# Kernel optimization log

Hardware: AMD Instinct MI355X
Metric: run time of the kernel (lower is better)

Reference implementation:

```python
import jax, jax.numpy as jnp
import numpy as np

ALPHA = 1.702  # gpt-oss gated-activation alpha
LIMIT = 7.0    # gpt-oss clamp limit
E, H, I = 8, 1024, 2048
B, S = 2, 2048


def setup_inputs() -> dict:
    key = jax.random.key(0)
    ks = jax.random.split(key, 6)
    return {
        "hidden_states": jax.random.normal(ks[0], (B, S, H), dtype=jnp.float32),
        "routing_weights": jax.random.uniform(ks[1], (B * S, E), dtype=jnp.float32),
        "gate_up_proj": jax.random.normal(ks[2], (E, H, 2 * I), dtype=jnp.float32) * 0.02,
        "gate_up_proj_bias": jax.random.normal(ks[3], (E, 2 * I), dtype=jnp.float32) * 0.02,
        "down_proj": jax.random.normal(ks[4], (E, I, H), dtype=jnp.float32) * 0.02,
        "down_proj_bias": jax.random.normal(ks[5], (E, H), dtype=jnp.float32) * 0.02,
    }


def reference(hidden_states, routing_weights, gate_up_proj, gate_up_proj_bias,
              down_proj, down_proj_bias):
    b, s, h = hidden_states.shape
    x = hidden_states.reshape(-1, h)  # [T, H]
    # all-experts dense path: [E, T, 2I]
    gate_up = jnp.einsum('th,ehd->etd', x, gate_up_proj) + gate_up_proj_bias[:, None, :]
    gate = gate_up[..., ::2]   # interleaved gate/up as in gpt-oss
    up = gate_up[..., 1::2]
    gate = jnp.minimum(gate, LIMIT)
    up = jnp.clip(up, -LIMIT, LIMIT)
    glu = gate * jax.nn.sigmoid(gate * ALPHA)
    # [E, T, H]
    out_e = jnp.einsum('eti,eih->eth', (up + 1.0) * glu, down_proj) + down_proj_bias[:, None, :]
    # weighted sum over experts with routing weights [T, E]
    out = jnp.einsum('eth,te->th', out_e, routing_weights)
    return out.reshape(b, s, h)
```

## Files before the change

### kernel.cpp

```cpp
#include <hip/hip_runtime.h>
#include <cstdint>

#define E_  8
#define H_  1024
#define I_  2048
#define T_  4096
#define D2_ 4096
#define K2_ 16384

typedef __bf16 bf16x8 __attribute__((ext_vector_type(8)));
typedef float  f32x4  __attribute__((ext_vector_type(4)));

__device__ __forceinline__ unsigned short f2bf(float f) {
  unsigned int u = __float_as_uint(f);
  u += 0x7FFFu + ((u >> 16) & 1u);
  return (unsigned short)(u >> 16);
}

__device__ __forceinline__ void gll16(const void* g, void* l) {
  __builtin_amdgcn_global_load_lds(
      (const __attribute__((address_space(1))) unsigned int*)(uintptr_t)g,
      (__attribute__((address_space(3))) unsigned int*)(uintptr_t)l,
      16, 0, 0);
}

#define BARX()  __builtin_amdgcn_s_barrier()
#define WLG()   { asm volatile("s_waitcnt lgkmcnt(0)" ::: "memory"); __builtin_amdgcn_sched_barrier(0); }
#define WVM4()  asm volatile("s_waitcnt vmcnt(4)" ::: "memory")
#define WVM0()  asm volatile("s_waitcnt vmcnt(0)" ::: "memory")

__global__ void cast_x_kernel(const float* __restrict__ x,
                              unsigned short* __restrict__ xb) {
  const int idx = (blockIdx.x * 256 + threadIdx.x) * 8;
  float4 a = *(const float4*)(x + idx);
  float4 b = *(const float4*)(x + idx + 4);
  unsigned short o[8];
  o[0]=f2bf(a.x); o[1]=f2bf(a.y); o[2]=f2bf(a.z); o[3]=f2bf(a.w);
  o[4]=f2bf(b.x); o[5]=f2bf(b.y); o[6]=f2bf(b.z); o[7]=f2bf(b.w);
  *(uint4*)(xb + idx) = *(const uint4*)o;
}

__global__ void transp_w1_kernel(const float* __restrict__ gup,
                                 unsigned short* __restrict__ w1g,
                                 unsigned short* __restrict__ w1u) {
  __shared__ float tile[64][65];
  const int h0 = blockIdx.x * 64;
  const int d0 = blockIdx.y * 64;
  const int e  = blockIdx.z;
  const int tid = threadIdx.x;
  const int r  = tid >> 4;
  const int c4 = (tid & 15) * 4;
  const float* src = gup + ((size_t)e * H_ + h0) * D2_ + d0;
#pragma unroll
  for (int c = 0; c < 4; ++c) {
    const int row = r + 16 * c;
    float4 v = *(const float4*)(src + (size_t)row * D2_ + c4);
    tile[row][c4+0] = v.x; tile[row][c4+1] = v.y;
    tile[row][c4+2] = v.z; tile[row][c4+3] = v.w;
  }
  __syncthreads();
  const int hl = tid & 63;
  const int jg = tid >> 6;
  const size_t jbase = (size_t)e * I_ + (d0 >> 1);
#pragma unroll
  for (int jj = 0; jj < 8; ++jj) {
    const int jl = jg * 8 + jj;
    w1g[(jbase + jl) * H_ + h0 + hl] = f2bf(tile[hl][2*jl]);
    w1u[(jbase + jl) * H_ + h0 + hl] = f2bf(tile[hl][2*jl+1]);
  }
}

__global__ void transp_w2_kernel(const float* __restrict__ dp,
                                 unsigned short* __restrict__ w2t) {
  __shared__ float tile[64][65];
  const int k0 = blockIdx.x * 64;
  const int h0 = blockIdx.y * 64;
  const int tid = threadIdx.x;
  const int r  = tid >> 4;
  const int c4 = (tid & 15) * 4;
#pragma unroll
  for (int c = 0; c < 4; ++c) {
    const int row = r + 16 * c;
    float4 v = *(const float4*)(dp + (size_t)(k0 + row) * H_ + h0 + c4);
    tile[row][c4+0] = v.x; tile[row][c4+1] = v.y;
    tile[row][c4+2] = v.z; tile[row][c4+3] = v.w;
  }
  __syncthreads();
  const int kl = tid & 63;
  const int hg = tid >> 6;
#pragma unroll
  for (int hh = 0; hh < 16; ++hh) {
    const int hl = hg * 16 + hh;
    w2t[(size_t)(h0 + hl) * K2_ + k0 + kl] = f2bf(tile[kl][hl]);
  }
}


#define STA1(B, HF, KT) {                                                    \
  _Pragma("unroll")                                                           \
  for (int ld = 0; ld < 2; ++ld) {                                            \
    const int r = rA + (HF)*64 + ld*128;                                      \
    gll16(Ag + (size_t)r * H_ + (KT)*64 + sg, &lds[B][r*64 + sl]);            \
  } }
#define STG1(B, KT) {                                                         \
  _Pragma("unroll")                                                           \
  for (int ld = 0; ld < 2; ++ld) {                                            \
    const int r = rA + ld*64;                                                 \
    gll16(Gg + (size_t)r * H_ + (KT)*64 + sg, &lds[B][16384 + r*64 + sl]);    \
  } }
#define STU1(B, KT) {                                                         \
  _Pragma("unroll")                                                           \
  for (int ld = 0; ld < 2; ++ld) {                                            \
    const int r = rA + ld*64;                                                 \
    gll16(Ug + (size_t)r * H_ + (KT)*64 + sg, &lds[B][24576 + r*64 + sl]);    \
  } }
#define LDA1(B, MH) {                                                         \
  _Pragma("unroll")                                                           \
  for (int m = 0; m < 4; ++m) {                                               \
    const int ro = (wm*128 + (MH)*64 + m*16 + arow) * 64;                     \
    av[m][0] = *(const bf16x8*)&lds[B][ro + sw0];                             \
    av[m][1] = *(const bf16x8*)&lds[B][ro + sw1];                             \
  } }
#define LDB1(B, DST, BASE) {                                                  \
  _Pragma("unroll")                                                           \
  for (int n = 0; n < 2; ++n) {                                               \
    const int ro = (BASE) + (wn*32 + n*16 + arow) * 64;                       \
    DST[n][0] = *(const bf16x8*)&lds[B][ro + sw0];                            \
    DST[n][1] = *(const bf16x8*)&lds[B][ro + sw1];                            \
  } }
#define MMA1(ACC, MH, BV)                                                     \
  __builtin_amdgcn_s_setprio(1);                                              \
  _Pragma("unroll")                                                           \
  for (int m = 0; m < 4; ++m)                                                 \
  _Pragma("unroll")                                                           \
  for (int n = 0; n < 2; ++n) {                                               \
    ACC[(MH)*4+m][n] = __builtin_amdgcn_mfma_f32_16x16x32_bf16(av[m][0], BV[n][0], ACC[(MH)*4+m][n], 0,0,0); \
    ACC[(MH)*4+m][n] = __builtin_amdgcn_mfma_f32_16x16x32_bf16(av[m][1], BV[n][1], ACC[(MH)*4+m][n], 0,0,0); \
  }                                                                           \
  __builtin_amdgcn_s_setprio(0);

#define NT1 16
#define TILE1(B, U) {                                                         \
    \
  LDA1(B, 0); LDB1(B, bgv, 16384); LDB1(B, buv, 24576);                       \
  if ((U)+1 < NT1) { STA1((B)^1, 1, (U)+1); STG1((B)^1, (U)+1); }             \
  WLG();                                                                      \
  MMA1(accg, 0, bgv); MMA1(accu, 0, buv);                                     \
  BARX();                                                                     \
   \
  LDA1(B, 1);                                                                 \
  if ((U)+2 < NT1) { STA1(B, 0, (U)+2); STU1(B, (U)+2); }                     \
  WLG();                                                                      \
  MMA1(accu, 1, buv); MMA1(accg, 1, bgv);                                     \
  if ((U)+2 < NT1) { WVM4(); } else { WVM0(); }                               \
  BARX();                                                                     \
}

__global__ __launch_bounds__(512, 2) void gemm1_act_kernel(
    const unsigned short* __restrict__ xb,
    const unsigned short* __restrict__ w1g,
    const unsigned short* __restrict__ w1u,
    const float* __restrict__ gub,
    const float* __restrict__ rw,
    unsigned short* __restrict__ actW)
{
  __shared__ unsigned short lds[2][32768];
  const int tid  = threadIdx.x;
  const int lane = tid & 63;
  const int wv   = tid >> 6;
  const int wm   = wv >> 2;
  const int wn   = wv & 3;

  const int L  = blockIdx.x + 16 * blockIdx.y;
  const int xk = L & 7, xs = L >> 3;
  const int t0 = ((xk >> 1) * 4 + (xs & 3)) * 256;
  const int j0 = ((xk & 1) * 8 + (xs >> 2)) * 128;
  const int e  = blockIdx.z;

  const int arow = lane & 15;
  const int q    = lane >> 4;
  const int sw0  = ((q    ) ^ (arow & 7)) * 8;
  const int sw1  = ((q + 4) ^ (arow & 7)) * 8;
  const int sg   = ((tid & 7) ^ ((tid >> 3) & 7)) * 8;
  const int sl   = (tid & 7) * 8;
  const int rA   = tid >> 3;

  const unsigned short* Ag = xb  + (size_t)t0 * H_;
  const unsigned short* Gg = w1g + ((size_t)e * I_ + j0) * H_;
  const unsigned short* Ug = w1u + ((size_t)e * I_ + j0) * H_;

  const f32x4 zero = {0.f, 0.f, 0.f, 0.f};
  f32x4 accg[8][2], accu[8][2];
#pragma unroll
  for (int m = 0; m < 8; ++m)
#pragma unroll
    for (int n = 0; n < 2; ++n) { accg[m][n] = zero; accu[m][n] = zero; }
  bf16x8 av[4][2], bgv[2][2], buv[2][2];

  STA1(0, 0, 0); STU1(0, 0); STA1(0, 1, 0); STG1(0, 0);
  STA1(1, 0, 1); STU1(1, 1);
  WVM4(); BARX();

#pragma unroll 1
  for (int t = 0; t < NT1; t += 2) {
    TILE1(0, t);
    TILE1(1, t+1);
  }

  const float* gbE = gub + (size_t)e * D2_;
#pragma unroll
  for (int n = 0; n < 2; ++n) {
    const int j = j0 + wn*32 + n*16 + arow;
    const float2 bgu = *(const float2*)&gbE[2*j];
#pragma unroll
    for (int mf = 0; mf < 8; ++mf) {
#pragma unroll
      for (int ri = 0; ri < 4; ++ri) {
        const int t = t0 + wm*128 + mf*16 + q*4 + ri;
        float g = accg[mf][n][ri] + bgu.x;
        float u = accu[mf][n][ri] + bgu.y;
        g = fminf(g, 7.0f);
        u = fminf(fmaxf(u, -7.0f), 7.0f);
        const float s   = 1.0f / (1.0f + __expf(-1.702f * g));
        const float val = (u + 1.0f) * (g * s) * rw[t * 8 + e];
        actW[(size_t)t * K2_ + e * I_ + j] = f2bf(val);
      }
    }
  }
}


#define STA2(B, HF, KT) {                                                    \
  _Pragma("unroll")                                                           \
  for (int ld = 0; ld < 2; ++ld) {                                            \
    const int r = rA + (HF)*64 + ld*128;                                      \
    gll16(Ag + (size_t)r * K2_ + (KT)*64 + sg, &lds[B][r*64 + sl]);           \
  } }
#define STB2(B, NH, KT) {                                                    \
  _Pragma("unroll")                                                           \
  for (int ld = 0; ld < 2; ++ld) {                                            \
    const int lr = rA + ld*64;                                                \
    const int r  = (lr & 31) + (NH)*32 + ((lr >> 5) << 6);                    \
    gll16(Bgp + (size_t)r * K2_ + (KT)*64 + sg, &lds[B][16384 + r*64 + sl]);  \
  } }
#define LDA2(B, MH) {                                                         \
  _Pragma("unroll")                                                           \
  for (int m = 0; m < 4; ++m) {                                               \
    const int ro = (wm*128 + (MH)*64 + m*16 + arow) * 64;                     \
    av[m][0] = *(const bf16x8*)&lds[B][ro + sw0];                             \
    av[m][1] = *(const bf16x8*)&lds[B][ro + sw1];                             \
  } }
#define LDB2(B, DST, NH) {                                                   \
  _Pragma("unroll")                                                           \
  for (int n = 0; n < 2; ++n) {                                               \
    const int ro = 16384 + (wn*64 + (NH)*32 + n*16 + arow) * 64;              \
    DST[n][0] = *(const bf16x8*)&lds[B][ro + sw0];                            \
    DST[n][1] = *(const bf16x8*)&lds[B][ro + sw1];                            \
  } }
#define MMA2(MH, NH, BV)                                                      \
  __builtin_amdgcn_s_setprio(1);                                              \
  _Pragma("unroll")                                                           \
  for (int m = 0; m < 4; ++m)                                                 \
  _Pragma("unroll")                                                           \
  for (int n = 0; n < 2; ++n) {                                               \
    acc[(MH)*4+m][(NH)*2+n] = __builtin_amdgcn_mfma_f32_16x16x32_bf16(av[m][0], BV[n][0], acc[(MH)*4+m][(NH)*2+n], 0,0,0); \
    acc[(MH)*4+m][(NH)*2+n] = __builtin_amdgcn_mfma_f32_16x16x32_bf16(av[m][1], BV[n][1], acc[(MH)*4+m][(NH)*2+n], 0,0,0); \
  }                                                                           \
  __builtin_amdgcn_s_setprio(0);

#define NT2 64
#define TILE2(B, U) {                                                         \
  LDA2(B, 0); LDB2(B, bv0, 0); LDB2(B, bv1, 1);                               \
  if ((U)+1 < NT2) { STA2((B)^1, 1, (U)+1); STB2((B)^1, 0, (U)+1); }          \
  WLG();                                                                      \
  MMA2(0, 0, bv0); MMA2(0, 1, bv1);                                           \
  BARX();                                                                     \
  LDA2(B, 1);                                                                 \
  if ((U)+2 < NT2) { STA2(B, 0, (U)+2); STB2(B, 1, (U)+2); }                  \
  WLG();                                                                      \
  MMA2(1, 1, bv1); MMA2(1, 0, bv0);                                           \
  if ((U)+2 < NT2) { WVM4(); } else { WVM0(); }                               \
  BARX();                                                                     \
}

__global__ __launch_bounds__(512, 2) void gemm2_kernel(
    const unsigned short* __restrict__ actW,
    const unsigned short* __restrict__ w2t,
    float* __restrict__ part)
{
  __shared__ unsigned short lds[2][32768];
  const int tid  = threadIdx.x;
  const int lane = tid & 63;
  const int wv   = tid >> 6;
  const int wm   = wv >> 2;
  const int wn   = wv & 3;

  const int L  = blockIdx.x + 16 * (blockIdx.y + 4 * blockIdx.z);
  const int xk = L & 7, xs = L >> 3;
  const int t0 = ((xk & 1) * 8 + (xs & 7)) * 256;
  const int h0 = (xs >> 3) * 256;
  const int cz = xk >> 1;
  const int c0 = cz * 4096;

  const int arow = lane & 15;
  const int q    = lane >> 4;
  const int sw0  = ((q    ) ^ (arow & 7)) * 8;
  const int sw1  = ((q + 4) ^ (arow & 7)) * 8;
  const int sg   = ((tid & 7) ^ ((tid >> 3) & 7)) * 8;
  const int sl   = (tid & 7) * 8;
  const int rA   = tid >> 3;

  const unsigned short* Ag  = actW + (size_t)t0 * K2_ + c0;
  const unsigned short* Bgp = w2t  + (size_t)h0 * K2_ + c0;

  const f32x4 zero = {0.f, 0.f, 0.f, 0.f};
  f32x4 acc[8][4];
#pragma unroll
  for (int m = 0; m < 8; ++m)
#pragma unroll
    for (int n = 0; n < 4; ++n) acc[m][n] = zero;
  bf16x8 av[4][2], bv0[2][2], bv1[2][2];

  STA2(0, 0, 0); STB2(0, 1, 0); STA2(0, 1, 0); STB2(0, 0, 0);
  STA2(1, 0, 1); STB2(1, 1, 1);
  WVM4(); BARX();

#pragma unroll 1
  for (int t = 0; t < NT2; t += 2) {
    TILE2(0, t);
    TILE2(1, t+1);
  }

  float* P = part + (size_t)cz * ((size_t)T_ * H_);
#pragma unroll
  for (int mf = 0; mf < 8; ++mf)
#pragma unroll
    for (int nf = 0; nf < 4; ++nf)
#pragma unroll
      for (int ri = 0; ri < 4; ++ri) {
        const int t = t0 + wm*128 + mf*16 + q*4 + ri;
        const int h = h0 + wn*64 + nf*16 + arow;
        P[(size_t)t * H_ + h] = acc[mf][nf][ri];
      }
}

__global__ void reduce_kernel(const float* __restrict__ part,
                              const float* __restrict__ rw,
                              const float* __restrict__ dpb,
                              float* __restrict__ out) {
  const int idx = blockIdx.x * 256 + threadIdx.x;
  const int t  = idx >> 8;
  const int hq = idx & 255;
  const float4* p = (const float4*)part;
  float4 v = p[idx];
  float4 a;
  a = p[idx + 1048576]; v.x += a.x; v.y += a.y; v.z += a.z; v.w += a.w;
  a = p[idx + 2097152]; v.x += a.x; v.y += a.y; v.z += a.z; v.w += a.w;
  a = p[idx + 3145728]; v.x += a.x; v.y += a.y; v.z += a.z; v.w += a.w;
  const float4 w0 = *(const float4*)(rw + t*8);
  const float4 w1 = *(const float4*)(rw + t*8 + 4);
  const float wgt[8] = {w0.x, w0.y, w0.z, w0.w, w1.x, w1.y, w1.z, w1.w};
  const float4* db = (const float4*)dpb;
#pragma unroll
  for (int e2 = 0; e2 < 8; ++e2) {
    float4 b = db[e2*256 + hq];
    v.x += wgt[e2]*b.x; v.y += wgt[e2]*b.y; v.z += wgt[e2]*b.z; v.w += wgt[e2]*b.w;
  }
  ((float4*)out)[idx] = v;
}

extern "C" void kernel_launch(void* const* d_in, const int* in_sizes, int n_in,
                              void* d_out, int out_size, void* d_ws, size_t ws_size,
                              hipStream_t stream) {
  const float* hs  = (const float*)d_in[0];
  const float* rw  = (const float*)d_in[1];
  const float* gup = (const float*)d_in[2];
  const float* gub = (const float*)d_in[3];
  const float* dp  = (const float*)d_in[4];
  const float* dpb = (const float*)d_in[5];
  float* out = (float*)d_out;

  char* ws = (char*)d_ws;
  unsigned short* xb   = (unsigned short*)(ws);
  unsigned short* w1g  = (unsigned short*)(ws + 8388608);
  unsigned short* w1u  = (unsigned short*)(ws + 41943040);
  float*          part = (float*)(ws + 8388608);
  unsigned short* w2t  = (unsigned short*)(ws + 75497472);
  unsigned short* actW = (unsigned short*)(ws + 109051904);

  hipLaunchKernelGGL(cast_x_kernel, dim3((T_ * H_) / 2048), dim3(256), 0, stream, hs, xb);
  hipLaunchKernelGGL(transp_w1_kernel, dim3(H_/64, D2_/64, E_), dim3(256), 0, stream, gup, w1g, w1u);
  hipLaunchKernelGGL(transp_w2_kernel, dim3(K2_/64, H_/64), dim3(256), 0, stream, dp, w2t);
  hipLaunchKernelGGL(gemm1_act_kernel, dim3(T_/256, I_/128, E_), dim3(512), 0, stream,
                     xb, w1g, w1u, gub, rw, actW);
  hipLaunchKernelGGL(gemm2_kernel, dim3(T_/256, H_/256, 4), dim3(512), 0, stream,
                     actW, w2t, part);
  hipLaunchKernelGGL(reduce_kernel, dim3((T_ * H_ / 4) / 256), dim3(256), 0, stream,
                     part, rw, dpb, out);
}
```

Measured before the change: 451.9 us.

## Simplify GEMM pipelines to one barrier per tile with whole-tile prefetch

Both GEMM main loops drop the interleaved half-tile prefetch scheme (two barriers per k-tile, prefetching two tiles ahead with vmcnt(4)). The new loop issues the full next tile's global-to-LDS loads at the top, runs both halves of the MMAs on the current buffer, then waits on vmcnt(0) and takes a single barrier. This cuts barrier and wait overhead but reduces prefetch depth to one tile. Global latency is now covered only by one tile's worth of MFMA work, which may expose memory stalls.

```diff
diff --git a/kernel.cpp b/kernel.cpp
--- a/kernel.cpp
+++ b/kernel.cpp
@@ -25,8 +25,8 @@
 }
 
 #define BARX()  __builtin_amdgcn_s_barrier()
-#define WLG()   { asm volatile("s_waitcnt lgkmcnt(0)" ::: "memory"); __builtin_amdgcn_sched_barrier(0); }
-#define WVM4()  asm volatile("s_waitcnt vmcnt(4)" ::: "memory")
+#define FENCE() __builtin_amdgcn_sched_barrier(0)
+#define LGK0()  asm volatile("s_waitcnt lgkmcnt(0)" ::: "memory")
 #define WVM0()  asm volatile("s_waitcnt vmcnt(0)" ::: "memory")
 
 __global__ void cast_x_kernel(const float* __restrict__ x,
@@ -141,19 +141,18 @@
 
 #define NT1 16
 #define TILE1(B, U) {                                                         \
-    \
+                \
+  if ((U)+1 < NT1) { STA1((B)^1, 0, (U)+1); STA1((B)^1, 1, (U)+1);            \
+                     STG1((B)^1, (U)+1);    STU1((B)^1, (U)+1); }             \
+  FENCE();                          \
   LDA1(B, 0); LDB1(B, bgv, 16384); LDB1(B, buv, 24576);                       \
-  if ((U)+1 < NT1) { STA1((B)^1, 1, (U)+1); STG1((B)^1, (U)+1); }             \
-  WLG();                                                                      \
   MMA1(accg, 0, bgv); MMA1(accu, 0, buv);                                     \
+  LDA1(B, 1);                                                                 \
+  MMA1(accu, 1, buv); MMA1(accg, 1, bgv);                                     \
+  LGK0();                      \
+  if ((U)+1 < NT1) WVM0();       \
   BARX();                                                                     \
-   \
-  LDA1(B, 1);                                                                 \
-  if ((U)+2 < NT1) { STA1(B, 0, (U)+2); STU1(B, (U)+2); }                     \
-  WLG();                                                                      \
-  MMA1(accu, 1, buv); MMA1(accg, 1, bgv);                                     \
-  if ((U)+2 < NT1) { WVM4(); } else { WVM0(); }                               \
-  BARX();                                                                     \
+  FENCE();                                   \
 }
 
 __global__ __launch_bounds__(512, 2) void gemm1_act_kernel(
@@ -197,9 +196,8 @@
     for (int n = 0; n < 2; ++n) { accg[m][n] = zero; accu[m][n] = zero; }
   bf16x8 av[4][2], bgv[2][2], buv[2][2];
 
-  STA1(0, 0, 0); STU1(0, 0); STA1(0, 1, 0); STG1(0, 0);
-  STA1(1, 0, 1); STU1(1, 1);
-  WVM4(); BARX();
+  STA1(0, 0, 0); STA1(0, 1, 0); STG1(0, 0); STU1(0, 0);
+  WVM0(); BARX(); FENCE();
 
 #pragma unroll 1
   for (int t = 0; t < NT1; t += 2) {
@@ -270,17 +268,17 @@
 
 #define NT2 64
 #define TILE2(B, U) {                                                         \
+  if ((U)+1 < NT2) { STA2((B)^1, 0, (U)+1); STA2((B)^1, 1, (U)+1);            \
+                     STB2((B)^1, 0, (U)+1); STB2((B)^1, 1, (U)+1); }          \
+  FENCE();                                                                    \
   LDA2(B, 0); LDB2(B, bv0, 0); LDB2(B, bv1, 1);                               \
-  if ((U)+1 < NT2) { STA2((B)^1, 1, (U)+1); STB2((B)^1, 0, (U)+1); }          \
-  WLG();                                                                      \
   MMA2(0, 0, bv0); MMA2(0, 1, bv1);                                           \
+  LDA2(B, 1);                                                                 \
+  MMA2(1, 0, bv0); MMA2(1, 1, bv1);                                           \
+  LGK0();                                                                     \
+  if ((U)+1 < NT2) WVM0();                                                    \
   BARX();                                                                     \
-  LDA2(B, 1);                                                                 \
-  if ((U)+2 < NT2) { STA2(B, 0, (U)+2); STB2(B, 1, (U)+2); }                  \
-  WLG();                                                                      \
-  MMA2(1, 1, bv1); MMA2(1, 0, bv0);                                           \
-  if ((U)+2 < NT2) { WVM4(); } else { WVM0(); }                               \
-  BARX();                                                                     \
+  FENCE();                                                                    \
 }
 
 __global__ __launch_bounds__(512, 2) void gemm2_kernel(
@@ -321,9 +319,8 @@
     for (int n = 0; n < 4; ++n) acc[m][n] = zero;
   bf16x8 av[4][2], bv0[2][2], bv1[2][2];
 
-  STA2(0, 0, 0); STB2(0, 1, 0); STA2(0, 1, 0); STB2(0, 0, 0);
-  STA2(1, 0, 1); STB2(1, 1, 1);
-  WVM4(); BARX();
+  STA2(0, 0, 0); STA2(0, 1, 0); STB2(0, 0, 0); STB2(0, 1, 0);
+  WVM0(); BARX(); FENCE();
 
 #pragma unroll 1
   for (int t = 0; t < NT2; t += 2) {
```

New measurement: 439.1 us. -2.8%, faster.
